# Kernel tuning notes

Measured on AMD Instinct MI355X. Metric: run time of the kernel, lower is better.

Reference implementation:

```python
import jax, jax.numpy as jnp
import numpy as np

H = 2048      # hidden_size
NH = 16       # num_heads
HD = H // NH  # head_dim
B, T = 2, 2048


def setup_inputs() -> dict:
    key = jax.random.key(0)
    ks = jax.random.split(key, 5)
    s = 1.0 / np.sqrt(H)
    return {
        "x": jax.random.normal(ks[0], (B, T, H), dtype=jnp.float32),
        "wq": jax.random.normal(ks[1], (H, H), dtype=jnp.float32) * s,
        "bq": jnp.zeros((H,), dtype=jnp.float32),
        "wk": jax.random.normal(ks[2], (H, H), dtype=jnp.float32) * s,
        "bk": jnp.zeros((H,), dtype=jnp.float32),
        "wv": jax.random.normal(ks[3], (H, H), dtype=jnp.float32) * s,
        "bv": jnp.zeros((H,), dtype=jnp.float32),
        "wo": jax.random.normal(ks[4], (H, H), dtype=jnp.float32) * s,
        "bo": jnp.zeros((H,), dtype=jnp.float32),
    }


def reference(x, wq, bq, wk, bk, wv, bv, wo, bo):
    Bx, Tx, C = x.shape
    # projections (torch Linear: x @ W.T + b)
    q = x @ wq.T + bq
    k = x @ wk.T + bk
    v = x @ wv.T + bv
    # [B, T, H] -> [B, NH, T, HD]
    q = q.reshape(Bx, Tx, NH, HD).transpose(0, 2, 1, 3)
    k = k.reshape(Bx, Tx, NH, HD).transpose(0, 2, 1, 3)
    v = v.reshape(Bx, Tx, NH, HD).transpose(0, 2, 1, 3)
    scale = 1.0 / np.sqrt(HD).astype(np.float32)
    scores = jnp.einsum('bhqd,bhkd->bhqk', q, k) * scale  # [B, NH, T, T]
    causal = jnp.tril(jnp.ones((Tx, Tx), dtype=bool))
    scores = jnp.where(causal[None, None], scores, -jnp.inf)
    attn = jax.nn.softmax(scores, axis=-1)
    out = jnp.einsum('bhqk,bhkd->bhqd', attn, v)  # [B, NH, T, HD]
    out = out.transpose(0, 2, 1, 3).reshape(Bx, Tx, C)
    return out @ wo.T + bo
```

## Files before the change

kernel.cpp:

```cpp
#include <hip/hip_runtime.h>
#include <stdint.h>

constexpr int H_  = 2048;
constexpr int NH_ = 16;
constexpr int HD_ = 128;
constexpr int B_  = 2;
constexpr int T_  = 2048;
constexpr int M_  = B_ * T_;

typedef unsigned short u16;
typedef __bf16 bf16x8 __attribute__((ext_vector_type(8)));
typedef float  f32x4  __attribute__((ext_vector_type(4)));

constexpr float C1_ = 0.08838834764831845f * 1.4426950408889634f;

template <int N> struct IC { static constexpr int value = N; };

__device__ __forceinline__ u16 f2bf(float f) {
  uint32_t u = __builtin_bit_cast(uint32_t, f);
  u += 0x7fffu + ((u >> 16) & 1u);
  return (u16)(u >> 16);
}

__device__ __forceinline__ uint32_t cvtpk(float lo, float hi) {
  uint32_t r;
  asm("v_cvt_pk_bf16_f32 %0, %1, %2" : "=v"(r) : "v"(lo), "v"(hi));
  return r;
}

__device__ __forceinline__ void gload_lds16(const void* g, void* lds) {
  auto gp = (const __attribute__((address_space(1))) uint32_t*)(uintptr_t)g;
  auto lp = (__attribute__((address_space(3))) uint32_t*)(uint32_t)(uintptr_t)lds;
  __builtin_amdgcn_global_load_lds(gp, lp, 16, 0, 0);
}

__device__ __forceinline__ f32x4 mfma16(bf16x8 a, bf16x8 b, f32x4 c) {
  return __builtin_amdgcn_mfma_f32_16x16x32_bf16(a, b, c, 0, 0, 0);
}

__global__ __launch_bounds__(512) void cvt5_kernel(
    const float4* __restrict__ x,  const float4* __restrict__ wq,
    const float4* __restrict__ wk, const float4* __restrict__ wv,
    const float4* __restrict__ wo, ushort4* __restrict__ dst) {
  const int bid = blockIdx.x, tid = threadIdx.x;
  const float4* src;
  size_t idx, dof;
  if (bid < 4096) {
    src = x; idx = (size_t)bid * 512 + tid; dof = 0;
  } else {
    int w = (bid - 4096) >> 11;
    int r = (bid - 4096) & 2047;
    idx = (size_t)r * 512 + tid;
    dof = 2097152u + (size_t)w * 1048576u;
    src = (w == 0) ? wq : (w == 1) ? wk : (w == 2) ? wv : wo;
  }
  float4 v = src[idx];
  ushort4 o;
  o.x = f2bf(v.x); o.y = f2bf(v.y); o.z = f2bf(v.z); o.w = f2bf(v.w);
  dst[dof + idx] = o;
}

__device__ __forceinline__ void gemm256_core(const u16* __restrict__ A,
                                             const u16* __restrict__ Bm,
                                             const float* __restrict__ bias,
                                             void* __restrict__ Cout,
                                             int bid, int outmode,
                                             float oscale) {
  __shared__ u16 As[3][256 * 64];
  __shared__ u16 Bs[3][128 * 64];
  constexpr int Kg = H_;
  constexpr int NT = Kg / 64;
  const int tid = threadIdx.x;
  const int wave = tid >> 6, lane = tid & 63, l15 = lane & 15, lhi = lane >> 4;
  const int tm = bid & 15, tn = bid >> 4;
  const int m0 = tm << 8, n0 = tn << 7;
  const int wr = wave >> 1, wc = wave & 1;

  f32x4 acc[4][4] = {};

  auto stageA = [&](int kt, int buf, int a) {
    int o = a * 8192 + tid * 16;
    int row = o >> 7;
    int sw = o ^ ((row & 7) << 4);
    int c8 = (sw >> 4) & 7;
    gload_lds16(A + (size_t)(m0 + row) * Kg + kt * 64 + c8 * 8,
                (char*)&As[buf][0] + a * 8192 + wave * 1024);
  };
  auto stageB = [&](int kt, int buf, int a) {
    int o = a * 8192 + tid * 16;
    int row = o >> 7;
    int sw = o ^ ((row & 7) << 4);
    int c8 = (sw >> 4) & 7;
    gload_lds16(Bm + (size_t)(n0 + row) * Kg + kt * 64 + c8 * 8,
                (char*)&Bs[buf][0] + a * 8192 + wave * 1024);
  };
  auto rdA = [&](int buf, int kk, int mi) -> bf16x8 {
    int row = wr * 64 + mi * 16 + l15;
    int ob = (row * 128 + kk * 64 + lhi * 16) ^ ((row & 7) << 4);
    return *(const bf16x8*)((const char*)&As[buf][0] + ob);
  };
  auto rdB = [&](int buf, int kk, int ni) -> bf16x8 {
    int row = wc * 64 + ni * 16 + l15;
    int ob = (row * 128 + kk * 64 + lhi * 16) ^ ((row & 7) << 4);
    return *(const bf16x8*)((const char*)&Bs[buf][0] + ob);
  };

  stageB(0, 0, 0); stageB(0, 0, 1);
  stageA(0, 0, 0); stageA(0, 0, 1); stageA(0, 0, 2); stageA(0, 0, 3);
  stageB(1, 1, 0); stageB(1, 1, 1);
  stageA(1, 1, 0); stageA(1, 1, 1); stageA(1, 1, 2); stageA(1, 1, 3);
  asm volatile("s_waitcnt vmcnt(6)" ::: "memory");
  __builtin_amdgcn_s_barrier();
  asm volatile("" ::: "memory");

  int cur = 0;
  for (int kt = 0; kt < NT; ++kt) {
    const bool hn2 = (kt + 2 < NT);
    const int nxt = (cur + 2 >= 3) ? cur - 1 : cur + 2;
    bf16x8 a0, a1, b0, b1, b2, b3;

    a0 = rdA(cur, 0, 0); a1 = rdA(cur, 0, 1);
    b0 = rdB(cur, 0, 0); b1 = rdB(cur, 0, 1);
    b2 = rdB(cur, 0, 2); b3 = rdB(cur, 0, 3);
    if (hn2) { stageB(kt + 2, nxt, 0); stageB(kt + 2, nxt, 1); }
    __builtin_amdgcn_s_barrier(); asm volatile("" ::: "memory");
    __builtin_amdgcn_s_setprio(1);
    acc[0][0] = mfma16(a0, b0, acc[0][0]); acc[0][1] = mfma16(a0, b1, acc[0][1]);
    acc[0][2] = mfma16(a0, b2, acc[0][2]); acc[0][3] = mfma16(a0, b3, acc[0][3]);
    acc[1][0] = mfma16(a1, b0, acc[1][0]); acc[1][1] = mfma16(a1, b1, acc[1][1]);
    acc[1][2] = mfma16(a1, b2, acc[1][2]); acc[1][3] = mfma16(a1, b3, acc[1][3]);
    __builtin_amdgcn_s_setprio(0);
    __builtin_amdgcn_s_barrier(); asm volatile("" ::: "memory");

    a0 = rdA(cur, 0, 2); a1 = rdA(cur, 0, 3);
    if (hn2) { stageA(kt + 2, nxt, 0); stageA(kt + 2, nxt, 1); }
    __builtin_amdgcn_s_barrier(); asm volatile("" ::: "memory");
    __builtin_amdgcn_s_setprio(1);
    acc[2][0] = mfma16(a0, b0, acc[2][0]); acc[2][1] = mfma16(a0, b1, acc[2][1]);
    acc[2][2] = mfma16(a0, b2, acc[2][2]); acc[2][3] = mfma16(a0, b3, acc[2][3]);
    acc[3][0] = mfma16(a1, b0, acc[3][0]); acc[3][1] = mfma16(a1, b1, acc[3][1]);
    acc[3][2] = mfma16(a1, b2, acc[3][2]); acc[3][3] = mfma16(a1, b3, acc[3][3]);
    __builtin_amdgcn_s_setprio(0);
    __builtin_amdgcn_s_barrier(); asm volatile("" ::: "memory");

    a0 = rdA(cur, 1, 0); a1 = rdA(cur, 1, 1);
    b0 = rdB(cur, 1, 0); b1 = rdB(cur, 1, 1);
    b2 = rdB(cur, 1, 2); b3 = rdB(cur, 1, 3);
    if (hn2) { stageA(kt + 2, nxt, 2); stageA(kt + 2, nxt, 3); }
    __builtin_amdgcn_s_barrier(); asm volatile("" ::: "memory");
    __builtin_amdgcn_s_setprio(1);
    acc[0][0] = mfma16(a0, b0, acc[0][0]); acc[0][1] = mfma16(a0, b1, acc[0][1]);
    acc[0][2] = mfma16(a0, b2, acc[0][2]); acc[0][3] = mfma16(a0, b3, acc[0][3]);
    acc[1][0] = mfma16(a1, b0, acc[1][0]); acc[1][1] = mfma16(a1, b1, acc[1][1]);
    acc[1][2] = mfma16(a1, b2, acc[1][2]); acc[1][3] = mfma16(a1, b3, acc[1][3]);
    __builtin_amdgcn_s_setprio(0);
    __builtin_amdgcn_s_barrier(); asm volatile("" ::: "memory");

    a0 = rdA(cur, 1, 2); a1 = rdA(cur, 1, 3);
    __builtin_amdgcn_s_barrier(); asm volatile("" ::: "memory");
    __builtin_amdgcn_s_setprio(1);
    acc[2][0] = mfma16(a0, b0, acc[2][0]); acc[2][1] = mfma16(a0, b1, acc[2][1]);
    acc[2][2] = mfma16(a0, b2, acc[2][2]); acc[2][3] = mfma16(a0, b3, acc[2][3]);
    acc[3][0] = mfma16(a1, b0, acc[3][0]); acc[3][1] = mfma16(a1, b1, acc[3][1]);
    acc[3][2] = mfma16(a1, b2, acc[3][2]); acc[3][3] = mfma16(a1, b3, acc[3][3]);
    __builtin_amdgcn_s_setprio(0);
    if (hn2)
      asm volatile("s_waitcnt vmcnt(6)" ::: "memory");
    else
      asm volatile("s_waitcnt vmcnt(0)" ::: "memory");
    __builtin_amdgcn_s_barrier(); asm volatile("" ::: "memory");
    cur = (cur == 2) ? 0 : cur + 1;
  }

  float bv[4];
#pragma unroll
  for (int ni = 0; ni < 4; ++ni) bv[ni] = bias[n0 + wc * 64 + ni * 16 + l15];

  if (outmode == 2) {
    const int b = m0 >> 11;
    const int tbase = (m0 & 2047) + wr * 64 + lhi * 4;
#pragma unroll
    for (int mi = 0; mi < 4; ++mi) {
#pragma unroll
      for (int ni = 0; ni < 4; ++ni) {
        int n = n0 + wc * 64 + ni * 16 + l15;
        ushort4 pk;
        pk.x = f2bf(acc[mi][ni][0] + bv[ni]);
        pk.y = f2bf(acc[mi][ni][1] + bv[ni]);
        pk.z = f2bf(acc[mi][ni][2] + bv[ni]);
        pk.w = f2bf(acc[mi][ni][3] + bv[ni]);
        *(ushort4*)((u16*)Cout + (size_t)(b * 2048 + n) * T_ + tbase +
                    mi * 16) = pk;
      }
    }
  } else {
#pragma unroll
    for (int mi = 0; mi < 4; ++mi) {
#pragma unroll
      for (int ni = 0; ni < 4; ++ni) {
        int n = n0 + wc * 64 + ni * 16 + l15;
#pragma unroll
        for (int r = 0; r < 4; ++r) {
          int m = m0 + wr * 64 + mi * 16 + lhi * 4 + r;
          float v = (acc[mi][ni][r] + bv[ni]) * oscale;
          if (outmode == 1)
            ((float*)Cout)[(size_t)m * H_ + n] = v;
          else
            ((u16*)Cout)[(size_t)m * H_ + n] = f2bf(v);
        }
      }
    }
  }
}

template <int OUTMODE>
__global__ __launch_bounds__(512, 1) void gemm256_bt_k(
    const u16* __restrict__ A, const u16* __restrict__ Bm,
    const float* __restrict__ bias, void* __restrict__ Cout, float oscale) {
  gemm256_core(A, Bm, bias, Cout, blockIdx.x, OUTMODE, oscale);
}

__global__ __launch_bounds__(256, 2) void attn_kernel(
    const u16* __restrict__ Q, const u16* __restrict__ K,
    const u16* __restrict__ Vt, u16* __restrict__ ctx) {
  __shared__ u16 Ks[2][64 * 128];
  __shared__ u16 Vs[2][128 * 64];
  __shared__ u16 Ps[4][1024];

  const int tid = threadIdx.x, wave = tid >> 6, lane = tid & 63;
  const int l15 = lane & 15, lhi = lane >> 4;

  const int bid = blockIdx.x;
  const int xcd = bid & 7, idx = bid >> 3;
  const int bh = xcd * 4 + (idx & 3);
  const int qi = idx >> 2;
  const int b = bh >> 4, h = bh & 15;
  const int qb0 = qi, qb1 = 31 - qi;
  const int bt = qb0 + 1;

  const float THR = 11.5f;
  const float NI  = -__builtin_inff();

  auto stage = [&](auto bufc, int kv0) {
    constexpr int BUF = decltype(bufc)::value;
#pragma unroll
    for (int is = 0; is < 4; ++is) {
      {
        int o_ = is * 4096 + tid * 16;
        int row = o_ >> 8;
        int sw = o_ ^ (((o_ >> 8) & 7) << 4);
        int c8 = (sw >> 4) & 15;
        gload_lds16(K + (size_t)(b * T_ + kv0 + row) * H_ + h * HD_ + c8 * 8,
                    &Ks[BUF][0] + (is * 2048 + wave * 512));
      }
      {
        int o_ = is * 4096 + tid * 16;
        int row = o_ >> 7;
        int sw = o_ ^ (((o_ >> 7) & 7) << 4);
        int t8 = (sw >> 4) & 7;
        gload_lds16(Vt + (size_t)(bh * HD_ + row) * T_ + kv0 + t8 * 8,
                    &Vs[BUF][0] + (is * 4096 / 2 + wave * 512));
      }
    }
  };

  bf16x8 qc[4], qn[4];
  {
    const u16* q0p =
        Q + (size_t)(b * T_ + qb0 * 64 + wave * 16 + l15) * H_ + h * HD_ + lhi * 8;
    const u16* q1p =
        Q + (size_t)(b * T_ + qb1 * 64 + wave * 16 + l15) * H_ + h * HD_ + lhi * 8;
#pragma unroll
    for (int kk = 0; kk < 4; ++kk) {
      qc[kk] = *(const bf16x8*)(q0p + kk * 32);
      qn[kk] = *(const bf16x8*)(q1p + kk * 32);
    }
  }

  f32x4 o[8] = {};
  float m2 = NI, lr = 0.f;

  auto flushout = [&](int qtile) {
    float invo[4];
    float inv = 1.0f / lr;
#pragma unroll
    for (int r = 0; r < 4; ++r) invo[r] = __shfl(inv, lhi * 4 + r);
    int q0 = qtile * 64 + wave * 16;
#pragma unroll
    for (int dt = 0; dt < 8; ++dt)
#pragma unroll
      for (int r = 0; r < 4; ++r)
        ctx[(size_t)(b * T_ + q0 + lhi * 4 + r) * H_ + h * HD_ + dt * 16 +
            l15] = f2bf(o[dt][r] * invo[r]);
  };

  stage(IC<0>{}, 0);
  asm volatile("s_waitcnt vmcnt(0)" ::: "memory");
  __builtin_amdgcn_s_barrier();
  asm volatile("" ::: "memory");

  auto body = [&](int t, auto bufc) {
    constexpr int BUF = decltype(bufc)::value;
    if (t < 32) {
      int tn = t + 1;
      int kvn = ((tn >= bt) ? tn - bt : tn) * 64;
      stage(IC<BUF ^ 1>{}, kvn);
    }
    if (t == bt) {
      flushout(qb0);
#pragma unroll
      for (int dt = 0; dt < 8; ++dt) o[dt] = f32x4{0.f, 0.f, 0.f, 0.f};
      m2 = NI;
      lr = 0.f;
#pragma unroll
      for (int kk = 0; kk < 4; ++kk) qc[kk] = qn[kk];
    }
    if (t < 32)
      asm volatile("s_waitcnt vmcnt(8)" ::: "memory");
    else
      asm volatile("s_waitcnt vmcnt(0)" ::: "memory");
    __builtin_amdgcn_s_barrier();
    asm volatile("" ::: "memory");

    const int kvt = (t >= bt) ? t - bt : t;
    const int kv0 = kvt * 64;
    const int qtile = (t >= bt) ? qb1 : qb0;
    const int q0 = qtile * 64 + wave * 16;
    const int qrow = q0 + l15;

    f32x4 sv[4];
    __builtin_amdgcn_s_setprio(1);
#pragma unroll
    for (int kt = 0; kt < 4; ++kt) {
      f32x4 sacc = {0.f, 0.f, 0.f, 0.f};
#pragma unroll
      for (int kk = 0; kk < 4; ++kk) {
        int row = kt * 16 + l15;
        int ob = (row * 256 + kk * 64 + lhi * 16) ^ ((row & 7) << 4);
        bf16x8 kf = *(const bf16x8*)((const char*)&Ks[BUF][0] + ob);
        sacc = mfma16(kf, qc[kk], sacc);
      }
      sv[kt] = sacc;
    }
    __builtin_amdgcn_s_setprio(0);

    float pmax2;
    {
      float pm[4];
      const bool diag = (t == qb0) || (t == 32);
      if (diag) {
#pragma unroll
        for (int kt = 0; kt < 4; ++kt) {
          int key0 = kv0 + kt * 16 + lhi * 4;
#pragma unroll
          for (int r = 0; r < 4; ++r)
            sv[kt][r] = (key0 + r <= qrow) ? sv[kt][r] : NI;
          pm[kt] = fmaxf(fmaxf(sv[kt][0], sv[kt][1]),
                         fmaxf(sv[kt][2], sv[kt][3]));
        }
      } else {
#pragma unroll
        for (int kt = 0; kt < 4; ++kt)
          pm[kt] = fmaxf(fmaxf(sv[kt][0], sv[kt][1]),
                         fmaxf(sv[kt][2], sv[kt][3]));
      }
      pmax2 = fmaxf(fmaxf(pm[0], pm[1]), fmaxf(pm[2], pm[3]));
    }
    pmax2 = fmaxf(pmax2, __shfl_xor(pmax2, 16));
    pmax2 = fmaxf(pmax2, __shfl_xor(pmax2, 32));

    if (__any(pmax2 - m2 > THR)) {
      float mn = fmaxf(m2, pmax2);
      float al = exp2f(m2 - mn);
      m2 = mn;
      lr *= al;
      float alo[4];
#pragma unroll
      for (int r = 0; r < 4; ++r) alo[r] = __shfl(al, lhi * 4 + r);
#pragma unroll
      for (int dt = 0; dt < 8; ++dt)
#pragma unroll
        for (int r = 0; r < 4; ++r) o[dt][r] *= alo[r];
    }

    float rsk[4];
#pragma unroll
    for (int kt = 0; kt < 4; ++kt) {
#pragma unroll
      for (int r = 0; r < 4; ++r) sv[kt][r] = exp2f(sv[kt][r] - m2);
      rsk[kt] = (sv[kt][0] + sv[kt][1]) + (sv[kt][2] + sv[kt][3]);
    }
    float rs = (rsk[0] + rsk[1]) + (rsk[2] + rsk[3]);
    rs += __shfl_xor(rs, 16);
    rs += __shfl_xor(rs, 32);
    lr += rs;

#pragma unroll
    for (int kt = 0; kt < 4; ++kt) {
      int slot = kt * 2 + (lhi >> 1);
      uint2 pk;
      pk.x = cvtpk(sv[kt][0], sv[kt][1]);
      pk.y = cvtpk(sv[kt][2], sv[kt][3]);
      *(uint2*)&Ps[wave][slot * 128 + ((l15 * 8) ^ ((slot & 7) << 3)) +
                         (lhi & 1) * 4] = pk;
    }
    asm volatile("" ::: "memory");

    __builtin_amdgcn_s_setprio(1);
#pragma unroll
    for (int ks = 0; ks < 2; ++ks) {
      int slot = ks * 4 + lhi;
      bf16x8 pf = *(const bf16x8*)&Ps[wave][slot * 128 +
                                            ((l15 * 8) ^ ((slot & 7) << 3))];
#pragma unroll
      for (int dt = 0; dt < 8; ++dt) {
        int row = dt * 16 + l15;
        int ob = (row * 128 + ks * 64 + lhi * 16) ^ ((row & 7) << 4);
        bf16x8 vf = *(const bf16x8*)((const char*)&Vs[BUF][0] + ob);
        o[dt] = mfma16(pf, vf, o[dt]);
      }
    }
    __builtin_amdgcn_s_setprio(0);

    __builtin_amdgcn_s_barrier();
    asm volatile("" ::: "memory");
  };

#pragma unroll 1
  for (int t2 = 0; t2 < 32; t2 += 2) {
    body(t2, IC<0>{});
    body(t2 + 1, IC<1>{});
  }
  body(32, IC<0>{});
  flushout(qb1);
}

extern "C" void kernel_launch(void* const* d_in, const int* in_sizes, int n_in,
                              void* d_out, int out_size, void* d_ws,
                              size_t ws_size, hipStream_t stream) {
  const float* x  = (const float*)d_in[0];
  const float* wq = (const float*)d_in[1];
  const float* bq = (const float*)d_in[2];
  const float* wk = (const float*)d_in[3];
  const float* bk = (const float*)d_in[4];
  const float* wv = (const float*)d_in[5];
  const float* bv = (const float*)d_in[6];
  const float* wo = (const float*)d_in[7];
  const float* bo = (const float*)d_in[8];

  char* ws = (char*)d_ws;
  constexpr size_t SZ_X = (size_t)M_ * H_ * 2;
  constexpr size_t SZ_W = (size_t)H_ * H_ * 2;
  u16* xb  = (u16*)(ws);
  u16* wqb = (u16*)(ws + SZ_X);
  u16* wkb = (u16*)(ws + SZ_X + 1 * SZ_W);
  u16* wvb = (u16*)(ws + SZ_X + 2 * SZ_W);
  u16* wob = (u16*)(ws + SZ_X + 3 * SZ_W);
  u16* Qb  = (u16*)(ws + 1 * SZ_X + 4 * SZ_W);
  u16* Kb  = (u16*)(ws + 2 * SZ_X + 4 * SZ_W);
  u16* Vtb = (u16*)(ws + 3 * SZ_X + 4 * SZ_W);
  u16* ctx = xb;

  cvt5_kernel<<<12288, 512, 0, stream>>>((const float4*)x, (const float4*)wq,
                                         (const float4*)wk, (const float4*)wv,
                                         (const float4*)wo, (ushort4*)ws);

  gemm256_bt_k<0><<<256, 512, 0, stream>>>(xb, wqb, bq, Qb, C1_);
  gemm256_bt_k<0><<<256, 512, 0, stream>>>(xb, wkb, bk, Kb, 1.0f);
  gemm256_bt_k<2><<<256, 512, 0, stream>>>(xb, wvb, bv, Vtb, 1.0f);

  attn_kernel<<<512, 256, 0, stream>>>(Qb, Kb, Vtb, ctx);

  gemm256_bt_k<1><<<256, 512, 0, stream>>>(ctx, wob, bo, d_out, 1.0f);
}
```

Measured before the change: 242.6 us.

## Share K/V tiles between paired causal q-tiles in attention kernel

Each block now keeps two q-tiles (qb0 and qb1) resident, each with its own accumulator and softmax state. It walks the KV tiles once, up to qb1, so every staged K/V tile serves both q-tiles while t <= qb0, instead of loading the low tile's KV range twice. The qi index is also remapped so that work per block alternates across the blockIdx range, which may balance the load better. In exchange, register pressure roughly doubles for the o accumulators and Q fragments, which could hurt occupancy under launch_bounds(256,2).

```diff
diff --git a/kernel.cpp b/kernel.cpp
--- a/kernel.cpp
+++ b/kernel.cpp
@@ -233,10 +233,10 @@
   const int bid = blockIdx.x;
   const int xcd = bid & 7, idx = bid >> 3;
   const int bh = xcd * 4 + (idx & 3);
-  const int qi = idx >> 2;
+  const int qj = idx >> 2;
+  const int qi = (qj < 8) ? qj : 23 - qj;
   const int b = bh >> 4, h = bh & 15;
   const int qb0 = qi, qb1 = 31 - qi;
-  const int bt = qb0 + 1;
 
   const float THR = 11.5f;
   const float NI  = -__builtin_inff();
@@ -264,7 +264,7 @@
     }
   };
 
-  bf16x8 qc[4], qn[4];
+  bf16x8 qc0[4], qc1[4];
   {
     const u16* q0p =
         Q + (size_t)(b * T_ + qb0 * 64 + wave * 16 + l15) * H_ + h * HD_ + lhi * 8;
@@ -272,60 +272,17 @@
         Q + (size_t)(b * T_ + qb1 * 64 + wave * 16 + l15) * H_ + h * HD_ + lhi * 8;
 #pragma unroll
     for (int kk = 0; kk < 4; ++kk) {
-      qc[kk] = *(const bf16x8*)(q0p + kk * 32);
-      qn[kk] = *(const bf16x8*)(q1p + kk * 32);
+      qc0[kk] = *(const bf16x8*)(q0p + kk * 32);
+      qc1[kk] = *(const bf16x8*)(q1p + kk * 32);
     }
   }
 
-  f32x4 o[8] = {};
-  float m2 = NI, lr = 0.f;
-
-  auto flushout = [&](int qtile) {
-    float invo[4];
-    float inv = 1.0f / lr;
-#pragma unroll
-    for (int r = 0; r < 4; ++r) invo[r] = __shfl(inv, lhi * 4 + r);
-    int q0 = qtile * 64 + wave * 16;
-#pragma unroll
-    for (int dt = 0; dt < 8; ++dt)
-#pragma unroll
-      for (int r = 0; r < 4; ++r)
-        ctx[(size_t)(b * T_ + q0 + lhi * 4 + r) * H_ + h * HD_ + dt * 16 +
-            l15] = f2bf(o[dt][r] * invo[r]);
-  };
-
-  stage(IC<0>{}, 0);
-  asm volatile("s_waitcnt vmcnt(0)" ::: "memory");
-  __builtin_amdgcn_s_barrier();
-  asm volatile("" ::: "memory");
-
-  auto body = [&](int t, auto bufc) {
+  f32x4 o0[8] = {}, o1[8] = {};
+  float m20 = NI, lr0 = 0.f, m21 = NI, lr1 = 0.f;
+
+  auto comp = [&](f32x4 (&o)[8], float& m2, float& lr, bf16x8 (&qf)[4],
+                  int q0, bool diag, int kv0, auto bufc) {
     constexpr int BUF = decltype(bufc)::value;
-    if (t < 32) {
-      int tn = t + 1;
-      int kvn = ((tn >= bt) ? tn - bt : tn) * 64;
-      stage(IC<BUF ^ 1>{}, kvn);
-    }
-    if (t == bt) {
-      flushout(qb0);
-#pragma unroll
-      for (int dt = 0; dt < 8; ++dt) o[dt] = f32x4{0.f, 0.f, 0.f, 0.f};
-      m2 = NI;
-      lr = 0.f;
-#pragma unroll
-      for (int kk = 0; kk < 4; ++kk) qc[kk] = qn[kk];
-    }
-    if (t < 32)
-      asm volatile("s_waitcnt vmcnt(8)" ::: "memory");
-    else
-      asm volatile("s_waitcnt vmcnt(0)" ::: "memory");
-    __builtin_amdgcn_s_barrier();
-    asm volatile("" ::: "memory");
-
-    const int kvt = (t >= bt) ? t - bt : t;
-    const int kv0 = kvt * 64;
-    const int qtile = (t >= bt) ? qb1 : qb0;
-    const int q0 = qtile * 64 + wave * 16;
     const int qrow = q0 + l15;
 
     f32x4 sv[4];
@@ -338,7 +295,7 @@
         int row = kt * 16 + l15;
         int ob = (row * 256 + kk * 64 + lhi * 16) ^ ((row & 7) << 4);
         bf16x8 kf = *(const bf16x8*)((const char*)&Ks[BUF][0] + ob);
-        sacc = mfma16(kf, qc[kk], sacc);
+        sacc = mfma16(kf, qf[kk], sacc);
       }
       sv[kt] = sacc;
     }
@@ -347,7 +304,6 @@
     float pmax2;
     {
       float pm[4];
-      const bool diag = (t == qb0) || (t == 32);
       if (diag) {
 #pragma unroll
         for (int kt = 0; kt < 4; ++kt) {
@@ -421,18 +377,56 @@
       }
     }
     __builtin_amdgcn_s_setprio(0);
-
+    asm volatile("" ::: "memory");
+  };
+
+  auto flushout = [&](f32x4 (&o)[8], float lr, int qtile) {
+    float invo[4];
+    float inv = 1.0f / lr;
+#pragma unroll
+    for (int r = 0; r < 4; ++r) invo[r] = __shfl(inv, lhi * 4 + r);
+    int q0 = qtile * 64 + wave * 16;
+#pragma unroll
+    for (int dt = 0; dt < 8; ++dt)
+#pragma unroll
+      for (int r = 0; r < 4; ++r)
+        ctx[(size_t)(b * T_ + q0 + lhi * 4 + r) * H_ + h * HD_ + dt * 16 +
+            l15] = f2bf(o[dt][r] * invo[r]);
+  };
+
+  stage(IC<0>{}, 0);
+  asm volatile("s_waitcnt vmcnt(0)" ::: "memory");
+  __builtin_amdgcn_s_barrier();
+  asm volatile("" ::: "memory");
+
+  auto body = [&](int t, auto bufc) {
+    constexpr int BUF = decltype(bufc)::value;
+    if (t < qb1) stage(IC<BUF ^ 1>{}, (t + 1) * 64);
+    if (t < qb1)
+      asm volatile("s_waitcnt vmcnt(8)" ::: "memory");
+    else
+      asm volatile("s_waitcnt vmcnt(0)" ::: "memory");
     __builtin_amdgcn_s_barrier();
     asm volatile("" ::: "memory");
+
+    const int kv0 = t * 64;
+    comp(o1, m21, lr1, qc1, qb1 * 64 + wave * 16, t == qb1, kv0, bufc);
+    if (t <= qb0)
+      comp(o0, m20, lr0, qc0, qb0 * 64 + wave * 16, t == qb0, kv0, bufc);
+
+    __builtin_amdgcn_s_barrier();
+    asm volatile("" ::: "memory");
   };
 
 #pragma unroll 1
-  for (int t2 = 0; t2 < 32; t2 += 2) {
+  for (int t2 = 0; t2 + 1 <= qb1; t2 += 2) {
     body(t2, IC<0>{});
     body(t2 + 1, IC<1>{});
   }
-  body(32, IC<0>{});
-  flushout(qb1);
+  if ((qb1 & 1) == 0) body(qb1, IC<0>{});
+
+  flushout(o0, lr0, qb0);
+  flushout(o1, lr1, qb1);
 }
 
 extern "C" void kernel_launch(void* const* d_in, const int* in_sizes, int n_in,
```

After: 240.8 us. No clear change (-0.8%).
